# Kernel optimization log

Hardware: AMD Instinct MI355X
Metric: run time of the kernel (lower is better)

## Reference

```python
import jax, jax.numpy as jnp
import numpy as np

NUM_NEIGH = 6  # 5 + 1 hardcoded in PeerNet

def pr_transform(h, num_neigh=NUM_NEIGH):
    # h: [B, F]. For each feature column, replace each value by the mean of its
    # num_neigh nearest batch values (by absolute difference, self included).
    def per_feat(col):  # col: [B]
        dist = jnp.abs(col[:, None] - col[None, :])  # [B, B]
        _, idx = jax.lax.top_k(-dist, num_neigh)      # [B, k] nearest indices
        return jnp.mean(col[idx], axis=1)             # [B]
    # lax.map over features keeps peak memory at one [B,B] matrix at a time
    return jax.lax.map(per_feat, h.T).T


def setup_inputs() -> dict:
    key = jax.random.key(0)
    ks = jax.random.split(key, 9)
    B, D = 4096, 1024
    H1, H2, O = 128, 64, 2
    s = 0.02
    return {
        "x":   jax.random.normal(ks[0], (B, D), dtype=jnp.float32),
        "W1":  jax.random.normal(ks[1], (H1, D), dtype=jnp.float32) * s,
        "b1":  jnp.zeros((H1,), dtype=jnp.float32),
        "Wpr": jax.random.normal(ks[2], (H1, H1), dtype=jnp.float32) * s,
        "bpr": jnp.zeros((H1,), dtype=jnp.float32),
        "W2":  jax.random.normal(ks[3], (H2, H1), dtype=jnp.float32) * s,
        "b2":  jnp.zeros((H2,), dtype=jnp.float32),
        "Wo":  jax.random.normal(ks[4], (O, H2), dtype=jnp.float32) * s,
        "bo":  jnp.zeros((O,), dtype=jnp.float32),
    }


def reference(x, W1, b1, Wpr, bpr, W2, b2, Wo, bo):
    # hidden1 + relu (dropout = identity, eval mode)
    h1 = jax.nn.relu(x @ W1.T + b1)               # [B, 128]
    # PRLayer: per-feature kNN averaging over batch, then linear
    pr = pr_transform(h1)                          # [B, 128]
    pr = jax.nn.relu(pr @ Wpr.T + bpr)             # [B, 128]
    h2 = jax.nn.relu(pr @ W2.T + b2)               # [B, 64]
    out = h2 @ Wo.T + bo                           # [B, 2]
    return out
```

## Files before the change

kernel.cpp:

```cpp
#include <hip/hip_runtime.h>


#define NB   4096
#define DIN  1024
#define NH1  128
#define NH2  64

#define PAD(p) ((p) + ((p) >> 3))

typedef _Float16 f16x8 __attribute__((ext_vector_type(8)));
typedef _Float16 f16x4 __attribute__((ext_vector_type(4)));
typedef float    f32x4 __attribute__((ext_vector_type(4)));

__global__ __launch_bounds__(512) void gemm1_mfma(const float* __restrict__ x,
                                                  const float* __restrict__ W1,
                                                  const float* __restrict__ b1,
                                                  float* __restrict__ h1T)
{
    __shared__ _Float16 xhi[16 * 1032];
    __shared__ _Float16 xlo[16 * 1032];
    const int tid = threadIdx.x;
    const int m0  = blockIdx.x * 16;

    {
        const int r  = tid >> 5;
        const int kb = (tid & 31) * 4;
#pragma unroll
        for (int i = 0; i < 8; ++i) {
            const int k = kb + i * 128;
            const float4 v = *(const float4*)&x[(size_t)(m0 + r) * DIN + k];
            const _Float16 h0 = (_Float16)v.x, h1 = (_Float16)v.y;
            const _Float16 h2 = (_Float16)v.z, h3 = (_Float16)v.w;
            f16x4 hv = {h0, h1, h2, h3};
            f16x4 lv = {(_Float16)(v.x - (float)h0), (_Float16)(v.y - (float)h1),
                        (_Float16)(v.z - (float)h2), (_Float16)(v.w - (float)h3)};
            *(f16x4*)&xhi[r * 1032 + k] = hv;
            *(f16x4*)&xlo[r * 1032 + k] = lv;
        }
    }
    __syncthreads();

    const int lane = tid & 63;
    const int w    = tid >> 6;
    const int n0   = w * 16;
    const int fr   = lane & 15;
    const int fq   = lane >> 4;

    f32x4 acc = {0.f, 0.f, 0.f, 0.f};
    const float* __restrict__ wp = &W1[(size_t)(n0 + fr) * DIN + fq * 8];
    const _Float16* xh = &xhi[fr * 1032 + fq * 8];
    const _Float16* xl = &xlo[fr * 1032 + fq * 8];

#pragma unroll 4
    for (int ks = 0; ks < 32; ++ks) {
        const int k = ks * 32;
        const f16x8 ah = *(const f16x8*)&xh[k];
        const f16x8 al = *(const f16x8*)&xl[k];
        const float4 wa = *(const float4*)&wp[k];
        const float4 wb = *(const float4*)&wp[k + 4];
        const float wf[8] = {wa.x, wa.y, wa.z, wa.w, wb.x, wb.y, wb.z, wb.w};
        f16x8 bh, bl;
#pragma unroll
        for (int q = 0; q < 8; ++q) {
            const _Float16 h = (_Float16)wf[q];
            bh[q] = h;
            bl[q] = (_Float16)(wf[q] - (float)h);
        }
        acc = __builtin_amdgcn_mfma_f32_16x16x32_f16(ah, bh, acc, 0, 0, 0);
        acc = __builtin_amdgcn_mfma_f32_16x16x32_f16(ah, bl, acc, 0, 0, 0);
        acc = __builtin_amdgcn_mfma_f32_16x16x32_f16(al, bh, acc, 0, 0, 0);
    }

    const int n = n0 + fr;
    const float bv = b1[n];
    float4 o;
    o.x = fmaxf(acc[0] + bv, 0.f);
    o.y = fmaxf(acc[1] + bv, 0.f);
    o.z = fmaxf(acc[2] + bv, 0.f);
    o.w = fmaxf(acc[3] + bv, 0.f);
    *(float4*)&h1T[(size_t)n * NB + m0 + fq * 4] = o;
}

__global__ __launch_bounds__(512) void sort_window_kernel(const float* __restrict__ h1T,
                                                          float* __restrict__ prtT)
{
    __shared__ float s[PAD(NB - 1) + 2];
    __shared__ float r_[PAD(NB - 1) + 2];
    const int t    = threadIdx.x;
    const int col  = blockIdx.x >> 1;
    const int half = blockIdx.x & 1;
    const float* __restrict__ src = h1T + (size_t)col * NB;

    float v[8];
    {
        const float4 a = *(const float4*)&src[8 * t];
        const float4 b = *(const float4*)&src[8 * t + 4];
        v[0] = a.x; v[1] = a.y; v[2] = a.z; v[3] = a.w;
        v[4] = b.x; v[5] = b.y; v[6] = b.z; v[7] = b.w;
    }

#define CE(a, b, up)                                        \
    {                                                       \
        const float _x = v[a], _y = v[b];                   \
        v[a] = (up) ? fminf(_x, _y) : fmaxf(_x, _y);        \
        v[b] = (up) ? fmaxf(_x, _y) : fminf(_x, _y);        \
    }

    CE(0, 1, true); CE(2, 3, false); CE(4, 5, true); CE(6, 7, false);
    CE(0, 2, true);  CE(1, 3, true);  CE(4, 6, false); CE(5, 7, false);
    CE(0, 1, true);  CE(2, 3, true);  CE(4, 5, false); CE(6, 7, false);

#pragma unroll
    for (int k = 8; k <= 256; k <<= 1) {
        const bool up = (t & (k >> 3)) == 0;
#pragma unroll
        for (int j = k >> 1; j >= 8; j >>= 1) {
            const int  m       = j >> 3;
            const bool keepmin = (((t & m) == 0) == up);
#pragma unroll
            for (int q = 0; q < 8; ++q) {
                const float p = __shfl_xor(v[q], m);
                v[q] = keepmin ? fminf(v[q], p) : fmaxf(v[q], p);
            }
        }
        CE(0, 4, up); CE(1, 5, up); CE(2, 6, up); CE(3, 7, up);
        CE(0, 2, up); CE(1, 3, up); CE(4, 6, up); CE(5, 7, up);
        CE(0, 1, up); CE(2, 3, up); CE(4, 5, up); CE(6, 7, up);
    }

#pragma unroll
    for (int k = 512; k <= 4096; k <<= 1) {
        const bool up = (t & (k >> 3)) == 0;
#pragma unroll
        for (int j = k >> 1; j >= 512; j >>= 1) {
            __syncthreads();
            float4 w0 = {v[0], v[1], v[2], v[3]};
            float4 w1 = {v[4], v[5], v[6], v[7]};
            *(float4*)&s[9 * t]     = w0;
            *(float4*)&s[9 * t + 4] = w1;
            __syncthreads();
            const int tp = t ^ (j >> 3);
            const float4 pa = *(const float4*)&s[9 * tp];
            const float4 pb = *(const float4*)&s[9 * tp + 4];
            const bool keepmin = (((t & (j >> 3)) == 0) == up);
            const float p[8] = {pa.x, pa.y, pa.z, pa.w, pb.x, pb.y, pb.z, pb.w};
#pragma unroll
            for (int q = 0; q < 8; ++q)
                v[q] = keepmin ? fminf(v[q], p[q]) : fmaxf(v[q], p[q]);
        }
#pragma unroll
        for (int j = 256; j >= 8; j >>= 1) {
            const int  m       = j >> 3;
            const bool keepmin = (((t & m) == 0) == up);
#pragma unroll
            for (int q = 0; q < 8; ++q) {
                const float p = __shfl_xor(v[q], m);
                v[q] = keepmin ? fminf(v[q], p) : fmaxf(v[q], p);
            }
        }
        CE(0, 4, up); CE(1, 5, up); CE(2, 6, up); CE(3, 7, up);
        CE(0, 2, up); CE(1, 3, up); CE(4, 6, up); CE(5, 7, up);
        CE(0, 1, up); CE(2, 3, up); CE(4, 5, up); CE(6, 7, up);
    }
#undef CE

    __syncthreads();
    {
        float4 w0 = {v[0], v[1], v[2], v[3]};
        float4 w1 = {v[4], v[5], v[6], v[7]};
        *(float4*)&s[9 * t]     = w0;
        *(float4*)&s[9 * t + 4] = w1;
    }
    __syncthreads();

    if (v[7] == 0.0f) {
        const float4 z4 = {0.f, 0.f, 0.f, 0.f};
        *(float4*)&r_[9 * t]     = z4;
        *(float4*)&r_[9 * t + 4] = z4;
    } else {
        float rr[8];
#pragma unroll
        for (int q = 0; q < 8; ++q) {
            const int  p  = 8 * t + q;
            const float v0 = v[q];
            int l = p, h = p;
            float sum = v0;
#pragma unroll
            for (int it = 0; it < 5; ++it) {
                const int li = (l > 0) ? l - 1 : 0;
                const int ri = (h < NB - 1) ? h + 1 : NB - 1;
                const float sl = s[PAD(li)];
                const float sr = s[PAD(ri)];
                const float dl = (l > 0) ? (v0 - sl) : 1e30f;
                const float dr = (h < NB - 1) ? (sr - v0) : 1e30f;
                if (dl <= dr) { sum += sl; l = li; }
                else          { sum += sr; h = ri; }
            }
            rr[q] = sum * (1.0f / 6.0f);
        }
        const float4 r0 = {rr[0], rr[1], rr[2], rr[3]};
        const float4 r1 = {rr[4], rr[5], rr[6], rr[7]};
        *(float4*)&r_[9 * t]     = r0;
        *(float4*)&r_[9 * t + 4] = r1;
    }
    __syncthreads();

    const float z5 = s[PAD(5)];
    float v0[4];
    bool  zs[4];
    float key[4];
    int   lo[4], hi[4];
#pragma unroll
    for (int w = 0; w < 4; ++w) {
        const int e = half * 2048 + t + w * 512;
        v0[w]  = src[e];
        zs[w]  = (v0[w] == 0.0f) && (z5 == 0.0f);
        key[w] = zs[w] ? -1.0f : v0[w];
        lo[w]  = 0;
        hi[w]  = NB;
    }
#pragma unroll
    for (int step = 0; step < 12; ++step) {
#pragma unroll
        for (int w = 0; w < 4; ++w) {
            const int mid = (lo[w] + hi[w]) >> 1;
            const float sv = s[PAD(mid)];
            if (sv < key[w]) lo[w] = mid + 1; else hi[w] = mid;
        }
    }
#pragma unroll
    for (int w = 0; w < 4; ++w) {
        const int e = half * 2048 + t + w * 512;
        const float res = zs[w] ? 0.0f : r_[PAD(lo[w])];
        prtT[(size_t)col * NB + e] = res;
    }
}

__global__ __launch_bounds__(512) void tail_kernel(const float* __restrict__ AT,
                                                   const float* __restrict__ Wpr,
                                                   const float* __restrict__ bpr,
                                                   const float* __restrict__ W2,
                                                   const float* __restrict__ b2,
                                                   const float* __restrict__ Wo,
                                                   const float* __restrict__ bo,
                                                   float* __restrict__ out)
{
    __shared__ float As[NH1 * 17];
    __shared__ float Bs[NH1 * 132];
    __shared__ float Ps[16 * 132];
    __shared__ float Rs[32 * 32];
    const int tid = threadIdx.x;
    const int m0  = blockIdx.x * 16;

    {
        const int row = tid >> 2;
        const int f   = (tid & 3) * 4;
        const float4 v = *(const float4*)&AT[(size_t)row * NB + m0 + f];
        As[row * 17 + f + 0] = v.x;
        As[row * 17 + f + 1] = v.y;
        As[row * 17 + f + 2] = v.z;
        As[row * 17 + f + 3] = v.w;
    }
    {
        const int n  = tid >> 2;
        const int kb = (tid & 3) * 32;
#pragma unroll
        for (int i4 = 0; i4 < 8; ++i4) {
            const float4 v = *(const float4*)&Wpr[(size_t)n * NH1 + kb + i4 * 4];
            Bs[(kb + i4 * 4 + 0) * 132 + n] = v.x;
            Bs[(kb + i4 * 4 + 1) * 132 + n] = v.y;
            Bs[(kb + i4 * 4 + 2) * 132 + n] = v.z;
            Bs[(kb + i4 * 4 + 3) * 132 + n] = v.w;
        }
    }
    __syncthreads();

    const int m  = tid & 15;
    const int g  = tid >> 4;
    const int n0 = g * 4;

    float acc[4] = {0.f, 0.f, 0.f, 0.f};
#pragma unroll 8
    for (int kk = 0; kk < NH1; ++kk) {
        const float a  = As[kk * 17 + m];
        const float4 b = *(const float4*)&Bs[kk * 132 + n0];
        acc[0] = fmaf(a, b.x, acc[0]);
        acc[1] = fmaf(a, b.y, acc[1]);
        acc[2] = fmaf(a, b.z, acc[2]);
        acc[3] = fmaf(a, b.w, acc[3]);
    }
#pragma unroll
    for (int j = 0; j < 4; ++j)
        Ps[m * 132 + n0 + j] = fmaxf(acc[j] + bpr[n0 + j], 0.f);
    __syncthreads();

    {
        const int j2 = tid >> 3;
        const int nb = (tid & 7) * 16;
#pragma unroll
        for (int i4 = 0; i4 < 4; ++i4) {
            const float4 v = *(const float4*)&W2[(size_t)j2 * NH1 + nb + i4 * 4];
            Bs[(nb + i4 * 4 + 0) * 68 + j2] = v.x;
            Bs[(nb + i4 * 4 + 1) * 68 + j2] = v.y;
            Bs[(nb + i4 * 4 + 2) * 68 + j2] = v.z;
            Bs[(nb + i4 * 4 + 3) * 68 + j2] = v.w;
        }
    }
    __syncthreads();

    const int j0 = g * 2;
    float acc2[2] = {0.f, 0.f};
#pragma unroll 8
    for (int nn = 0; nn < NH1; ++nn) {
        const float p  = Ps[m * 132 + nn];
        const float2 w = *(const float2*)&Bs[nn * 68 + j0];
        acc2[0] = fmaf(p, w.x, acc2[0]);
        acc2[1] = fmaf(p, w.y, acc2[1]);
    }

    float po0 = 0.f, po1 = 0.f;
#pragma unroll
    for (int j = 0; j < 2; ++j) {
        const float h = fmaxf(acc2[j] + b2[j0 + j], 0.f);
        po0 = fmaf(h, Wo[j0 + j], po0);
        po1 = fmaf(h, Wo[NH2 + j0 + j], po1);
    }
    Rs[g * 32 + m * 2 + 0] = po0;
    Rs[g * 32 + m * 2 + 1] = po1;
    __syncthreads();
    if (tid < 32) {
        const int mm = tid >> 1, o = tid & 1;
        float sum = 0.f;
#pragma unroll
        for (int gg = 0; gg < 32; ++gg) sum += Rs[gg * 32 + mm * 2 + o];
        out[(size_t)(m0 + mm) * 2 + o] = sum + bo[o];
    }
}

extern "C" void kernel_launch(void* const* d_in, const int* in_sizes, int n_in,
                              void* d_out, int out_size, void* d_ws, size_t ws_size,
                              hipStream_t stream)
{
    const float* x   = (const float*)d_in[0];
    const float* W1  = (const float*)d_in[1];
    const float* b1  = (const float*)d_in[2];
    const float* Wpr = (const float*)d_in[3];
    const float* bpr = (const float*)d_in[4];
    const float* W2  = (const float*)d_in[5];
    const float* b2  = (const float*)d_in[6];
    const float* Wo  = (const float*)d_in[7];
    const float* bo  = (const float*)d_in[8];

    float* ws     = (float*)d_ws;
    float* h1T    = ws;
    float* prtT   = h1T + NH1 * NB;

    gemm1_mfma<<<dim3(NB / 16), 512, 0, stream>>>(x, W1, b1, h1T);
    sort_window_kernel<<<dim3(NH1 * 2), 512, 0, stream>>>(h1T, prtT);
    tail_kernel<<<dim3(NB / 16), 512, 0, stream>>>(prtT, Wpr, bpr, W2, b2, Wo, bo,
                                                   (float*)d_out);
}
```

Baseline: 52.56 us.

## Move tail MLP GEMMs to split-fp16 MFMA with packed hi/lo activations

Rewrites the tail kernel so both the Wpr and W2 matmuls run on 16x16x32 fp16 MFMA instructions. A three-term hi/lo split keeps accuracy close to fp32. Activations are stored in shared memory as packed hi/lo halves, and weights are read straight from global memory and split in registers instead of being transposed through LDS. This removes the scalar FMA loops and the large weight staging buffer. In exchange it adds conversion work, runs the second GEMM on only 4 of 8 waves, and lengthens the final reduction to 64 partial sums.

```diff
diff --git a/kernel.cpp b/kernel.cpp
--- a/kernel.cpp
+++ b/kernel.cpp
@@ -11,6 +11,29 @@
 typedef _Float16 f16x8 __attribute__((ext_vector_type(8)));
 typedef _Float16 f16x4 __attribute__((ext_vector_type(4)));
 typedef float    f32x4 __attribute__((ext_vector_type(4)));
+
+__device__ __forceinline__ unsigned pack_hl(float x) {
+    const _Float16 h = (_Float16)x;
+    const _Float16 l = (_Float16)(x - (float)h);
+    unsigned short hu, lu;
+    __builtin_memcpy(&hu, &h, 2);
+    __builtin_memcpy(&lu, &l, 2);
+    return (unsigned)hu | ((unsigned)lu << 16);
+}
+
+__device__ __forceinline__ void unpack8(const unsigned* __restrict__ p,
+                                        f16x8& hv, f16x8& lv) {
+#pragma unroll
+    for (int q = 0; q < 8; ++q) {
+        const unsigned u = p[q];
+        const unsigned short hu = (unsigned short)(u & 0xffffu);
+        const unsigned short lu = (unsigned short)(u >> 16);
+        _Float16 h, l;
+        __builtin_memcpy(&h, &hu, 2);
+        __builtin_memcpy(&l, &lu, 2);
+        hv[q] = h; lv[q] = l;
+    }
+}
 
 __global__ __launch_bounds__(512) void gemm1_mfma(const float* __restrict__ x,
                                                   const float* __restrict__ W1,
@@ -245,94 +268,106 @@
                                                    const float* __restrict__ bo,
                                                    float* __restrict__ out)
 {
-    __shared__ float As[NH1 * 17];
-    __shared__ float Bs[NH1 * 132];
-    __shared__ float Ps[16 * 132];
-    __shared__ float Rs[32 * 32];
+    __shared__ unsigned Apk[16 * 132];
+    __shared__ unsigned Ppk[16 * 132];
+    __shared__ float    Rs[64 * 32];
     const int tid = threadIdx.x;
     const int m0  = blockIdx.x * 16;
 
     {
-        const int row = tid >> 2;
-        const int f   = (tid & 3) * 4;
-        const float4 v = *(const float4*)&AT[(size_t)row * NB + m0 + f];
-        As[row * 17 + f + 0] = v.x;
-        As[row * 17 + f + 1] = v.y;
-        As[row * 17 + f + 2] = v.z;
-        As[row * 17 + f + 3] = v.w;
-    }
-    {
-        const int n  = tid >> 2;
-        const int kb = (tid & 3) * 32;
-#pragma unroll
-        for (int i4 = 0; i4 < 8; ++i4) {
-            const float4 v = *(const float4*)&Wpr[(size_t)n * NH1 + kb + i4 * 4];
-            Bs[(kb + i4 * 4 + 0) * 132 + n] = v.x;
-            Bs[(kb + i4 * 4 + 1) * 132 + n] = v.y;
-            Bs[(kb + i4 * 4 + 2) * 132 + n] = v.z;
-            Bs[(kb + i4 * 4 + 3) * 132 + n] = v.w;
-        }
-    }
-    __syncthreads();
-
-    const int m  = tid & 15;
-    const int g  = tid >> 4;
-    const int n0 = g * 4;
-
-    float acc[4] = {0.f, 0.f, 0.f, 0.f};
-#pragma unroll 8
-    for (int kk = 0; kk < NH1; ++kk) {
-        const float a  = As[kk * 17 + m];
-        const float4 b = *(const float4*)&Bs[kk * 132 + n0];
-        acc[0] = fmaf(a, b.x, acc[0]);
-        acc[1] = fmaf(a, b.y, acc[1]);
-        acc[2] = fmaf(a, b.z, acc[2]);
-        acc[3] = fmaf(a, b.w, acc[3]);
-    }
-#pragma unroll
-    for (int j = 0; j < 4; ++j)
-        Ps[m * 132 + n0 + j] = fmaxf(acc[j] + bpr[n0 + j], 0.f);
-    __syncthreads();
-
-    {
-        const int j2 = tid >> 3;
-        const int nb = (tid & 7) * 16;
-#pragma unroll
-        for (int i4 = 0; i4 < 4; ++i4) {
-            const float4 v = *(const float4*)&W2[(size_t)j2 * NH1 + nb + i4 * 4];
-            Bs[(nb + i4 * 4 + 0) * 68 + j2] = v.x;
-            Bs[(nb + i4 * 4 + 1) * 68 + j2] = v.y;
-            Bs[(nb + i4 * 4 + 2) * 68 + j2] = v.z;
-            Bs[(nb + i4 * 4 + 3) * 68 + j2] = v.w;
-        }
-    }
-    __syncthreads();
-
-    const int j0 = g * 2;
-    float acc2[2] = {0.f, 0.f};
-#pragma unroll 8
-    for (int nn = 0; nn < NH1; ++nn) {
-        const float p  = Ps[m * 132 + nn];
-        const float2 w = *(const float2*)&Bs[nn * 68 + j0];
-        acc2[0] = fmaf(p, w.x, acc2[0]);
-        acc2[1] = fmaf(p, w.y, acc2[1]);
-    }
-
-    float po0 = 0.f, po1 = 0.f;
-#pragma unroll
-    for (int j = 0; j < 2; ++j) {
-        const float h = fmaxf(acc2[j] + b2[j0 + j], 0.f);
-        po0 = fmaf(h, Wo[j0 + j], po0);
-        po1 = fmaf(h, Wo[NH2 + j0 + j], po1);
-    }
-    Rs[g * 32 + m * 2 + 0] = po0;
-    Rs[g * 32 + m * 2 + 1] = po1;
-    __syncthreads();
+        const int k = tid >> 2;
+        const int f = (tid & 3) * 4;
+        const float4 v = *(const float4*)&AT[(size_t)k * NB + m0 + f];
+        const float vf[4] = {v.x, v.y, v.z, v.w};
+#pragma unroll
+        for (int j = 0; j < 4; ++j)
+            Apk[(f + j) * 132 + k] = pack_hl(vf[j]);
+    }
+    __syncthreads();
+
+    const int lane = tid & 63;
+    const int w    = tid >> 6;
+    const int fr   = lane & 15;
+    const int fq   = lane >> 4;
+
+    {
+        const int n0 = w * 16;
+        f32x4 acc = {0.f, 0.f, 0.f, 0.f};
+        const float*    __restrict__ wp = &Wpr[(size_t)(n0 + fr) * NH1 + fq * 8];
+        const unsigned* __restrict__ ap = &Apk[fr * 132 + fq * 8];
+#pragma unroll
+        for (int ks = 0; ks < 4; ++ks) {
+            const int k = ks * 32;
+            f16x8 ah, al;
+            unpack8(&ap[k], ah, al);
+            const float4 wa = *(const float4*)&wp[k];
+            const float4 wb = *(const float4*)&wp[k + 4];
+            const float wf[8] = {wa.x, wa.y, wa.z, wa.w, wb.x, wb.y, wb.z, wb.w};
+            f16x8 bh, bl;
+#pragma unroll
+            for (int q = 0; q < 8; ++q) {
+                const _Float16 h = (_Float16)wf[q];
+                bh[q] = h;
+                bl[q] = (_Float16)(wf[q] - (float)h);
+            }
+            acc = __builtin_amdgcn_mfma_f32_16x16x32_f16(ah, bh, acc, 0, 0, 0);
+            acc = __builtin_amdgcn_mfma_f32_16x16x32_f16(ah, bl, acc, 0, 0, 0);
+            acc = __builtin_amdgcn_mfma_f32_16x16x32_f16(al, bh, acc, 0, 0, 0);
+        }
+        const int n = n0 + fr;
+        const float bv = bpr[n];
+#pragma unroll
+        for (int j = 0; j < 4; ++j) {
+            const float p = fmaxf(acc[j] + bv, 0.f);
+            Ppk[(fq * 4 + j) * 132 + n] = pack_hl(p);
+        }
+    }
+    __syncthreads();
+
+    if (w < 4) {
+        const int j0 = w * 16;
+        f32x4 acc2 = {0.f, 0.f, 0.f, 0.f};
+        const float*    __restrict__ w2p = &W2[(size_t)(j0 + fr) * NH1 + fq * 8];
+        const unsigned* __restrict__ pp  = &Ppk[fr * 132 + fq * 8];
+#pragma unroll
+        for (int ks = 0; ks < 4; ++ks) {
+            const int k = ks * 32;
+            f16x8 ah, al;
+            unpack8(&pp[k], ah, al);
+            const float4 wa = *(const float4*)&w2p[k];
+            const float4 wb = *(const float4*)&w2p[k + 4];
+            const float wf[8] = {wa.x, wa.y, wa.z, wa.w, wb.x, wb.y, wb.z, wb.w};
+            f16x8 bh, bl;
+#pragma unroll
+            for (int q = 0; q < 8; ++q) {
+                const _Float16 h = (_Float16)wf[q];
+                bh[q] = h;
+                bl[q] = (_Float16)(wf[q] - (float)h);
+            }
+            acc2 = __builtin_amdgcn_mfma_f32_16x16x32_f16(ah, bh, acc2, 0, 0, 0);
+            acc2 = __builtin_amdgcn_mfma_f32_16x16x32_f16(ah, bl, acc2, 0, 0, 0);
+            acc2 = __builtin_amdgcn_mfma_f32_16x16x32_f16(al, bh, acc2, 0, 0, 0);
+        }
+        const int jj  = j0 + fr;
+        const float b2v = b2[jj];
+        const float wo0 = Wo[jj];
+        const float wo1 = Wo[NH2 + jj];
+        const int g = w * 16 + fr;
+#pragma unroll
+        for (int j = 0; j < 4; ++j) {
+            const float h = fmaxf(acc2[j] + b2v, 0.f);
+            const int m = fq * 4 + j;
+            Rs[g * 32 + m * 2 + 0] = h * wo0;
+            Rs[g * 32 + m * 2 + 1] = h * wo1;
+        }
+    }
+    __syncthreads();
+
     if (tid < 32) {
         const int mm = tid >> 1, o = tid & 1;
         float sum = 0.f;
 #pragma unroll
-        for (int gg = 0; gg < 32; ++gg) sum += Rs[gg * 32 + mm * 2 + o];
+        for (int g = 0; g < 64; ++g) sum += Rs[g * 32 + mm * 2 + o];
         out[(size_t)(m0 + mm) * 2 + o] = sum + bo[o];
     }
 }
```

Result: faster. 47.27 us (median of 2 runs) (-10.1%).
